# Optimization experiments

Measured on AMD Instinct MI355X. Metric: run time of the kernel, lower is better.

The kernel has to match this reference:

```python
import jax, jax.numpy as jnp
import numpy as np

B, S, H, DH = 8, 2048, 4, 32
D = H * DH  # all_head_size = true_hidden_size = 128


def setup_inputs() -> dict:
    key = jax.random.key(0)
    ks = jax.random.split(key, 9)
    inp = {
        "query_tensor": jax.random.normal(ks[0], (B, S, D), dtype=jnp.float32),
        "key_tensor": jax.random.normal(ks[1], (B, S, D), dtype=jnp.float32),
        "value_tensor": jax.random.normal(ks[2], (B, S, D), dtype=jnp.float32),
        "attention_mask": jnp.zeros((B, 1, 1, S), dtype=jnp.float32),
        "head_mask": jnp.ones((1, H, 1, 1), dtype=jnp.float32),
        "Wq": jax.random.normal(ks[3], (D, D), dtype=jnp.float32) * 0.02,
        "bq": jnp.zeros((D,), dtype=jnp.float32),
        "Wk": jax.random.normal(ks[4], (D, D), dtype=jnp.float32) * 0.02,
        "bk": jnp.zeros((D,), dtype=jnp.float32),
        "Wv": jax.random.normal(ks[5], (D, D), dtype=jnp.float32) * 0.02,
        "bv": jnp.zeros((D,), dtype=jnp.float32),
    }
    return inp


def _split_heads(x):
    # (B, S, D) -> (B, H, S, DH)
    return x.reshape(B, S, H, DH).transpose(0, 2, 1, 3)


def reference(query_tensor, key_tensor, value_tensor, attention_mask, head_mask,
              Wq, bq, Wk, bk, Wv, bv):
    q = _split_heads(query_tensor @ Wq + bq)   # (B,H,S,DH)
    k = _split_heads(key_tensor @ Wk + bk)
    v = _split_heads(value_tensor @ Wv + bv)

    scale = 1.0 / jnp.sqrt(jnp.float32(DH))
    scores = jnp.einsum("bhqd,bhkd->bhqk", q, k) * scale + attention_mask
    probs = jax.nn.softmax(scores, axis=-1)
    # dropout is identity at inference (training=False)
    probs = probs * head_mask
    ctx = jnp.einsum("bhqk,bhkd->bhqd", probs, v)  # (B,H,S,DH)
    ctx = ctx.transpose(0, 2, 1, 3).reshape(B, S, D)
    return ctx
```

## Files before the change

### kernel.cpp

```cpp
#include <hip/hip_runtime.h>
#include <hip/hip_bf16.h>
#include <math.h>

#define B_ 8
#define S_ 2048
#define H_ 4
#define DH_ 32
#define D_ 128
#define BS_ (B_ * S_)
#define LOG2E 1.4426950408889634f
#define QSCALE (0.17677669529663687f * LOG2E)

typedef float f32x4  __attribute__((ext_vector_type(4)));
typedef float f32x16 __attribute__((ext_vector_type(16)));
typedef short s16x8  __attribute__((ext_vector_type(8)));

__device__ __forceinline__ unsigned short bf(float x) {
    return __builtin_bit_cast(unsigned short, __float2bfloat16(x));
}
__device__ __forceinline__ float bf2f(unsigned short u) {
    return __builtin_bit_cast(float, (unsigned int)u << 16);
}
__device__ __forceinline__ unsigned int pk2(float a, float b) {
    unsigned int r;
    asm("v_cvt_pk_bf16_f32 %0, %1, %2" : "=v"(r) : "v"(a), "v"(b));
    return r;
}
__device__ __forceinline__ void pswap(unsigned int& a, unsigned int& b) {
    asm volatile("v_permlane32_swap_b32 %0, %1" : "+v"(a), "+v"(b));
}
__device__ __forceinline__ void gll16(const void* g, void* l) {
    __builtin_amdgcn_global_load_lds(
        (const __attribute__((address_space(1))) unsigned int*)(g),
        (__attribute__((address_space(3))) unsigned int*)(l), 16, 0, 0);
}

#define OFF_Q  0u
#define OFF_K  2097152u
#define OFF_V  4194304u
#define OFF_W  6291456u
#define OFF_E  6389760u

__global__ __launch_bounds__(256) void wprep(
    const float* __restrict__ Wq, const float* __restrict__ Wk, const float* __restrict__ Wv,
    const float* __restrict__ maskg,
    unsigned short* __restrict__ Wt, unsigned short* __restrict__ Em)
{
    if (blockIdx.z == 3) {
        const int id16 = blockIdx.y * 4 + blockIdx.x;
        const int base = id16 * 1024 + threadIdx.x * 4;
        float4 m4 = *(const float4*)&maskg[base];
        ushort4 o;
        o.x = bf(__builtin_amdgcn_exp2f(m4.x * LOG2E));
        o.y = bf(__builtin_amdgcn_exp2f(m4.y * LOG2E));
        o.z = bf(__builtin_amdgcn_exp2f(m4.z * LOG2E));
        o.w = bf(__builtin_amdgcn_exp2f(m4.w * LOG2E));
        *(ushort4*)&Em[base] = o;
        return;
    }
    const float* W = (blockIdx.z == 0) ? Wq : (blockIdx.z == 1) ? Wk : Wv;
    unsigned short* Oh = Wt + (size_t)blockIdx.z * D_ * D_;
    unsigned short* Ol = Oh + 3 * D_ * D_;
    __shared__ float tf[32][36];
    const int t = threadIdx.x;
    const int kt = blockIdx.x * 32, ct = blockIdx.y * 32;
    {
        int kl = t >> 3, cl = (t & 7) * 4;
        float4 w4 = *(const float4*)&W[(size_t)(kt + kl) * D_ + ct + cl];
        tf[kl][cl + 0] = w4.x; tf[kl][cl + 1] = w4.y;
        tf[kl][cl + 2] = w4.z; tf[kl][cl + 3] = w4.w;
    }
    __syncthreads();
    {
        int cl = t >> 3, kl = (t & 7) * 4;
        ushort4 oh, ol;
        float v;
        v = tf[kl + 0][cl]; oh.x = bf(v); ol.x = bf(v - bf2f(oh.x));
        v = tf[kl + 1][cl]; oh.y = bf(v); ol.y = bf(v - bf2f(oh.y));
        v = tf[kl + 2][cl]; oh.z = bf(v); ol.z = bf(v - bf2f(oh.z));
        v = tf[kl + 3][cl]; oh.w = bf(v); ol.w = bf(v - bf2f(oh.w));
        *(ushort4*)&Oh[(size_t)(ct + cl) * D_ + kt + kl] = oh;
        *(ushort4*)&Ol[(size_t)(ct + cl) * D_ + kt + kl] = ol;
    }
}

__global__ __launch_bounds__(256) void qkv_mfma(
    const float* __restrict__ Xq, const float* __restrict__ Xk, const float* __restrict__ Xv,
    const unsigned short* __restrict__ Wt, const float* __restrict__ maskg,
    const float* __restrict__ bq, const float* __restrict__ bk, const float* __restrict__ bv,
    unsigned short* __restrict__ Qo, unsigned short* __restrict__ Kf,
    unsigned short* __restrict__ Vf)
{
    const int mode = blockIdx.z, chalf = blockIdx.y;
    const float* X; const float* bias; float scl;
    if (mode == 0)      { X = Xq; bias = bq; scl = QSCALE; }
    else if (mode == 1) { X = Xk; bias = bk; scl = 1.f; }
    else                { X = Xv; bias = bv; scl = 1.f; }
    const unsigned short* WmH = Wt + (size_t)mode * D_ * D_;
    const unsigned short* WmL = WmH + 3 * D_ * D_;

    __shared__ __align__(16) unsigned short xa[2 * 32 * 136];
    __shared__ __align__(16) unsigned short wt[2 * 64 * 136];

    const int t = threadIdx.x;
    const int w = t >> 6, lane = t & 63, lo = lane & 15, hi = lane >> 4;
    const int mf = w >> 1, nb = (w & 1) * 2;

    #pragma unroll
    for (int j = 0; j < 8; j++) {
        int idx = t + 256 * j;
        int part = idx >> 10, i2 = idx & 1023;
        int r = i2 >> 4, c16 = i2 & 15;
        const unsigned short* src = part ? WmL : WmH;
        uint4 v = *(const uint4*)&src[(size_t)(chalf * 64 + r) * D_ + c16 * 8];
        *(uint4*)&wt[part * 8704 + r * 136 + c16 * 8] = v;
    }

    for (int rt = 0; rt < 4; rt++) {
        const long row0 = ((long)blockIdx.x * 4 + rt) * 32;

        __syncthreads();
        #pragma unroll
        for (int j = 0; j < 4; j++) {
            int idx = t + 256 * j;
            int r = idx >> 5, c4 = idx & 31;
            float4 v = *(const float4*)(X + (row0 + r) * D_ + c4 * 4);
            ushort4 ph, pl;
            ph.x = bf(v.x); pl.x = bf(v.x - bf2f(ph.x));
            ph.y = bf(v.y); pl.y = bf(v.y - bf2f(ph.y));
            ph.z = bf(v.z); pl.z = bf(v.z - bf2f(ph.z));
            ph.w = bf(v.w); pl.w = bf(v.w - bf2f(ph.w));
            *(ushort4*)&xa[r * 136 + c4 * 4] = ph;
            *(ushort4*)&xa[4352 + r * 136 + c4 * 4] = pl;
        }
        __syncthreads();

        f32x4 acc[2] = {};
        #pragma unroll
        for (int kk = 0; kk < 4; kk++) {
            const int ko = kk * 32 + hi * 8;
            s16x8 ah = *(const s16x8*)&xa[(mf * 16 + lo) * 136 + ko];
            s16x8 al = *(const s16x8*)&xa[4352 + (mf * 16 + lo) * 136 + ko];
            #pragma unroll
            for (int n2 = 0; n2 < 2; n2++) {
                const int nf = nb + n2;
                s16x8 bh2 = *(const s16x8*)&wt[(nf * 16 + lo) * 136 + ko];
                s16x8 bl2 = *(const s16x8*)&wt[8704 + (nf * 16 + lo) * 136 + ko];
                acc[n2] = __builtin_amdgcn_mfma_f32_16x16x32_bf16(ah, bh2, acc[n2], 0, 0, 0);
                acc[n2] = __builtin_amdgcn_mfma_f32_16x16x32_bf16(al, bh2, acc[n2], 0, 0, 0);
                acc[n2] = __builtin_amdgcn_mfma_f32_16x16x32_bf16(ah, bl2, acc[n2], 0, 0, 0);
            }
        }
        __syncthreads();

        const long b_i = row0 >> 11;
        const long s0g = row0 & 2047;

        if (mode < 2) {
            #pragma unroll
            for (int n2 = 0; n2 < 2; n2++) {
                int c_l = (nb + n2) * 16 + lo;
                float bb = bias[chalf * 64 + c_l];
                #pragma unroll
                for (int r = 0; r < 4; r++) {
                    int s = mf * 16 + hi * 4 + r;
                    xa[s * 72 + c_l] = bf((acc[n2][r] + bb) * scl);
                }
            }
            __syncthreads();
            int s = t >> 3, part = t & 7;
            int c_g = chalf * 64 + part * 8;
            int h = c_g >> 5, dd = c_g & 31;
            long s_i = s0g + s;
            int bh = (int)(b_i * H_ + h);
            uint4 val = *(const uint4*)&xa[s * 72 + part * 8];
            if (mode == 0) {
                *(uint4*)(Qo + ((size_t)bh * S_ + s_i) * DH_ + dd) = val;
            } else {
                int fr = dd >> 4, hwd = (dd >> 3) & 1;
                size_t off = ((((size_t)bh * 64 + (s_i >> 5)) * 2 + fr) * 64
                              + (s_i & 31) + hwd * 32) * 8;
                *(uint4*)(Kf + off) = val;
            }
        } else {
            float emr[4];
            #pragma unroll
            for (int r = 0; r < 4; r++) {
                const int s_l = mf * 16 + hi * 4 + r;
                emr[r] = __builtin_amdgcn_exp2f(maskg[b_i * S_ + s0g + s_l] * LOG2E);
            }
            #pragma unroll
            for (int n2 = 0; n2 < 2; n2++) {
                int c_l = (nb + n2) * 16 + lo;
                float bb = bias[chalf * 64 + c_l];
                #pragma unroll
                for (int r = 0; r < 4; r++) {
                    int s = mf * 16 + hi * 4 + r;
                    xa[c_l * 68 + s] = bf((acc[n2][r] + bb) * emr[r]);
                }
            }
            __syncthreads();
            if (t < 128) {
                int c_l = t >> 1, sh2 = (t & 1) * 16;
                int c_g = chalf * 64 + c_l;
                int h = c_g >> 5, dd = c_g & 31;
                long key0 = s0g + sh2;
                int bh = (int)(b_i * H_ + h);
                size_t base = (((size_t)bh * 128 + (key0 >> 4)) * 64 + dd) * 8;
                uint2 p0 = *(const uint2*)&xa[c_l * 68 + sh2 + 0];
                uint2 p1 = *(const uint2*)&xa[c_l * 68 + sh2 + 4];
                uint2 p2 = *(const uint2*)&xa[c_l * 68 + sh2 + 8];
                uint2 p3 = *(const uint2*)&xa[c_l * 68 + sh2 + 12];
                *(uint4*)(Vf + base)       = make_uint4(p0.x, p0.y, p1.x, p1.y);
                *(uint4*)(Vf + base + 256) = make_uint4(p2.x, p2.y, p3.x, p3.y);
            }
        }
    }
}

__global__ __launch_bounds__(512) void flash_mfma(
    const unsigned short* __restrict__ Qg, const unsigned short* __restrict__ Kfg,
    const unsigned short* __restrict__ Vfg, const unsigned short* __restrict__ Emg,
    const float* __restrict__ head_mask, float* __restrict__ Out)
{
    __shared__ __align__(16) unsigned short smem[26624];

    const int t = threadIdx.x, w = t >> 6, lane = t & 63;
    const int l31 = lane & 31, hw = lane >> 5;
    const int kq = w & 3, qh = w >> 2;

    const int lid = blockIdx.x;
    const int xcd = lid & 7, ser = lid >> 3;
    const int bh = xcd * 4 + (ser >> 5);
    const int qi = ser & 31;
    const int b = bh >> 2, h = bh & 3;
    const int q0 = qi * 64 + qh * 32;

    *(uint2*)&smem[24576 + t * 4] = *(const uint2*)(Emg + (size_t)b * S_ + t * 4);

    const unsigned short* qp = Qg + ((size_t)bh * S_ + q0 + l31) * DH_ + hw * 8;
    const s16x8 qf0 = *(const s16x8*)qp;
    const s16x8 qf1 = *(const s16x8*)(qp + 16);

    const size_t kvbase = (size_t)bh * 65536;
    const unsigned short* ksrc = Kfg + kvbase + (size_t)w * 512 + (size_t)lane * 8;
    const unsigned short* vsrc = Vfg + kvbase + (size_t)w * 512 + (size_t)lane * 8;

    #pragma unroll
    for (int p = 0; p < 3; p++) {
        gll16(ksrc + (size_t)p * 4096, &smem[p * 4096 + w * 512]);
        gll16(vsrc + (size_t)p * 4096, &smem[12288 + p * 4096 + w * 512]);
    }
    __syncthreads();

    const unsigned short* emb = &smem[24576];
    f32x16 ctx = {}, lacc = {};
    const f32x16 z16 = {};

    s16x8 vf_cur0, vf_cur1, ef_cur0, ef_cur1;
    f32x16 s_cur;
    {
        const unsigned short* kb = &smem[kq * 1024];
        const unsigned short* vb = &smem[12288 + kq * 1024];
        s16x8 k0 = *(const s16x8*)(kb + (size_t)lane * 8);
        s16x8 k1 = *(const s16x8*)(kb + 512 + (size_t)lane * 8);
        vf_cur0 = *(const s16x8*)(vb + (size_t)lane * 8);
        vf_cur1 = *(const s16x8*)(vb + 512 + (size_t)lane * 8);
        ef_cur0 = *(const s16x8*)(emb + kq * 32 + hw * 8);
        ef_cur1 = *(const s16x8*)(emb + kq * 32 + hw * 8 + 16);
        s_cur = __builtin_amdgcn_mfma_f32_32x32x16_bf16(k0, qf0, z16, 0, 0, 0);
        s_cur = __builtin_amdgcn_mfma_f32_32x32x16_bf16(k1, qf1, s_cur, 0, 0, 0);
    }

    #pragma unroll
    for (int tile = 0; tile < 16; tile++) {
        if (tile < 14)       { asm volatile("s_waitcnt vmcnt(2)" ::: "memory"); }
        else if (tile == 14) { asm volatile("s_waitcnt vmcnt(0)" ::: "memory"); }
        __builtin_amdgcn_sched_barrier(0);
        __builtin_amdgcn_s_barrier();
        __builtin_amdgcn_sched_barrier(0);

        f32x16 s_next;
        s16x8 vf_n0, vf_n1, ef_n0, ef_n1;
        if (tile < 15) {
            const int nb3 = ((tile + 1) % 3) * 4096 + kq * 1024;
            const unsigned short* kb = &smem[nb3];
            const unsigned short* vb = &smem[12288 + nb3];
            s16x8 kn0 = *(const s16x8*)(kb + (size_t)lane * 8);
            s16x8 kn1 = *(const s16x8*)(kb + 512 + (size_t)lane * 8);
            vf_n0 = *(const s16x8*)(vb + (size_t)lane * 8);
            vf_n1 = *(const s16x8*)(vb + 512 + (size_t)lane * 8);
            ef_n0 = *(const s16x8*)(emb + (tile + 1) * 128 + kq * 32 + hw * 8);
            ef_n1 = *(const s16x8*)(emb + (tile + 1) * 128 + kq * 32 + hw * 8 + 16);
            s_next = __builtin_amdgcn_mfma_f32_32x32x16_bf16(kn0, qf0, z16, 0, 0, 0);
            s_next = __builtin_amdgcn_mfma_f32_32x32x16_bf16(kn1, qf1, s_next, 0, 0, 0);

            if (tile <= 12) {
                gll16(ksrc + (size_t)(tile + 3) * 4096, &smem[(tile % 3) * 4096 + w * 512]);
                gll16(vsrc + (size_t)(tile + 3) * 4096, &smem[12288 + (tile % 3) * 4096 + w * 512]);
            }
        }

        unsigned int pd[8];
        #pragma unroll
        for (int j = 0; j < 8; j++) {
            pd[j] = pk2(__builtin_amdgcn_exp2f(s_cur[2 * j]),
                        __builtin_amdgcn_exp2f(s_cur[2 * j + 1]));
        }
        pswap(pd[0], pd[2]); pswap(pd[1], pd[3]);
        pswap(pd[4], pd[6]); pswap(pd[5], pd[7]);
        const s16x8 pa0 = __builtin_bit_cast(s16x8, make_uint4(pd[0], pd[1], pd[2], pd[3]));
        const s16x8 pa1 = __builtin_bit_cast(s16x8, make_uint4(pd[4], pd[5], pd[6], pd[7]));

        ctx  = __builtin_amdgcn_mfma_f32_32x32x16_bf16(pa0, vf_cur0, ctx, 0, 0, 0);
        lacc = __builtin_amdgcn_mfma_f32_32x32x16_bf16(pa0, ef_cur0, lacc, 0, 0, 0);
        ctx  = __builtin_amdgcn_mfma_f32_32x32x16_bf16(pa1, vf_cur1, ctx, 0, 0, 0);
        lacc = __builtin_amdgcn_mfma_f32_32x32x16_bf16(pa1, ef_cur1, lacc, 0, 0, 0);

        if (tile < 15) {
            s_cur = s_next;
            vf_cur0 = vf_n0; vf_cur1 = vf_n1;
            ef_cur0 = ef_n0; ef_cur1 = ef_n1;
        }
    }

    __syncthreads();
    float* ms = (float*)smem;
    #define MS(qh_, sl_, ln_, r_) ms[(((qh_) * 2 + (sl_)) * 64 + (ln_)) * 33 + (r_)]

    if (kq >= 2) {
        #pragma unroll
        for (int r = 0; r < 16; r++) {
            MS(qh, kq - 2, lane, r) = ctx[r];
            MS(qh, kq - 2, lane, 16 + r) = lacc[r];
        }
    }
    __syncthreads();
    if (kq < 2) {
        #pragma unroll
        for (int r = 0; r < 16; r++) {
            ctx[r]  += MS(qh, kq, lane, r);
            lacc[r] += MS(qh, kq, lane, 16 + r);
        }
    }
    __syncthreads();
    if (kq == 1) {
        #pragma unroll
        for (int r = 0; r < 16; r++) {
            MS(qh, 0, lane, r) = ctx[r];
            MS(qh, 0, lane, 16 + r) = lacc[r];
        }
    }
    __syncthreads();
    if (kq == 0) {
        #pragma unroll
        for (int r = 0; r < 16; r++) {
            ctx[r]  += MS(qh, 0, lane, r);
            lacc[r] += MS(qh, 0, lane, 16 + r);
        }
        const float hm = head_mask[h];
        #pragma unroll
        for (int r = 0; r < 16; r++) {
            const int qrow = (r & 3) + 8 * (r >> 2) + 4 * hw;
            Out[((size_t)b * S_ + q0 + qrow) * D_ + h * DH_ + l31] = ctx[r] * hm / lacc[r];
        }
    }
    #undef MS
}

extern "C" void kernel_launch(void* const* d_in, const int* in_sizes, int n_in,
                              void* d_out, int out_size, void* d_ws, size_t ws_size,
                              hipStream_t stream) {
    const float* Xq   = (const float*)d_in[0];
    const float* Xk   = (const float*)d_in[1];
    const float* Xv   = (const float*)d_in[2];
    const float* mask = (const float*)d_in[3];
    const float* hm   = (const float*)d_in[4];
    const float* Wq   = (const float*)d_in[5];
    const float* bq   = (const float*)d_in[6];
    const float* Wk   = (const float*)d_in[7];
    const float* bk   = (const float*)d_in[8];
    const float* Wv   = (const float*)d_in[9];
    const float* bv   = (const float*)d_in[10];
    float* out = (float*)d_out;

    unsigned short* ws = (unsigned short*)d_ws;
    unsigned short* Qo = ws + OFF_Q;
    unsigned short* Kf = ws + OFF_K;
    unsigned short* Vf = ws + OFF_V;
    unsigned short* Wt = ws + OFF_W;
    unsigned short* Em = ws + OFF_E;

    wprep<<<dim3(4, 4, 4), 256, 0, stream>>>(Wq, Wk, Wv, mask, Wt, Em);
    qkv_mfma<<<dim3(128, 2, 3), 256, 0, stream>>>(Xq, Xk, Xv, Wt, mask,
                                                  bq, bk, bv, Qo, Kf, Vf);
    flash_mfma<<<dim3(1024), 512, 0, stream>>>(Qo, Kf, Vf, Em, hm, out);
}
```

Before: 52.68 us.

## Rebalance flash kernel to 4 query groups x 2 key splits per block

Changes the flash attention block decomposition from 2 query subgroups x 4 key-split waves to 4 query subgroups x 2 key-split waves, so each block covers 128 queries and the grid halves to 512 blocks. Each K/V tile staged in shared memory is now reused by twice as many query rows, which halves global K/V traffic per output and cuts LDS use. The cross-wave reduction drops from two stages to one. In exchange, each wave runs twice as many key tiles (32) in a loop that is no longer unrolled, and there are fewer blocks to fill the GPU.

```diff
diff --git a/kernel.cpp b/kernel.cpp
--- a/kernel.cpp
+++ b/kernel.cpp
@@ -223,37 +223,37 @@
     const unsigned short* __restrict__ Vfg, const unsigned short* __restrict__ Emg,
     const float* __restrict__ head_mask, float* __restrict__ Out)
 {
-    __shared__ __align__(16) unsigned short smem[26624];
+    __shared__ __align__(16) unsigned short smem[16896];
 
     const int t = threadIdx.x, w = t >> 6, lane = t & 63;
     const int l31 = lane & 31, hw = lane >> 5;
-    const int kq = w & 3, qh = w >> 2;
+    const int kq = w & 1, qh = w >> 1;
 
     const int lid = blockIdx.x;
     const int xcd = lid & 7, ser = lid >> 3;
-    const int bh = xcd * 4 + (ser >> 5);
-    const int qi = ser & 31;
+    const int bh = xcd * 4 + (ser >> 4);
+    const int qi = ser & 15;
     const int b = bh >> 2, h = bh & 3;
-    const int q0 = qi * 64 + qh * 32;
-
-    *(uint2*)&smem[24576 + t * 4] = *(const uint2*)(Emg + (size_t)b * S_ + t * 4);
+    const int q0 = qi * 128 + qh * 32;
+
+    *(uint2*)&smem[12288 + t * 4] = *(const uint2*)(Emg + (size_t)b * S_ + t * 4);
 
     const unsigned short* qp = Qg + ((size_t)bh * S_ + q0 + l31) * DH_ + hw * 8;
     const s16x8 qf0 = *(const s16x8*)qp;
     const s16x8 qf1 = *(const s16x8*)(qp + 16);
 
     const size_t kvbase = (size_t)bh * 65536;
-    const unsigned short* ksrc = Kfg + kvbase + (size_t)w * 512 + (size_t)lane * 8;
-    const unsigned short* vsrc = Vfg + kvbase + (size_t)w * 512 + (size_t)lane * 8;
+    const int schunk = w & 3;
+    const unsigned short* ssrc = ((w < 4) ? Kfg : Vfg) + kvbase
+                               + (size_t)schunk * 512 + (size_t)lane * 8;
+    const int sdst = ((w < 4) ? 0 : 6144) + schunk * 512;
 
     #pragma unroll
-    for (int p = 0; p < 3; p++) {
-        gll16(ksrc + (size_t)p * 4096, &smem[p * 4096 + w * 512]);
-        gll16(vsrc + (size_t)p * 4096, &smem[12288 + p * 4096 + w * 512]);
-    }
+    for (int p = 0; p < 3; p++)
+        gll16(ssrc + (size_t)p * 2048, &smem[p * 2048 + sdst]);
     __syncthreads();
 
-    const unsigned short* emb = &smem[24576];
+    const unsigned short* emb = &smem[12288];
     f32x16 ctx = {}, lacc = {};
     const f32x16 z16 = {};
 
@@ -261,7 +261,7 @@
     f32x16 s_cur;
     {
         const unsigned short* kb = &smem[kq * 1024];
-        const unsigned short* vb = &smem[12288 + kq * 1024];
+        const unsigned short* vb = &smem[6144 + kq * 1024];
         s16x8 k0 = *(const s16x8*)(kb + (size_t)lane * 8);
         s16x8 k1 = *(const s16x8*)(kb + 512 + (size_t)lane * 8);
         vf_cur0 = *(const s16x8*)(vb + (size_t)lane * 8);
@@ -272,33 +272,30 @@
         s_cur = __builtin_amdgcn_mfma_f32_32x32x16_bf16(k1, qf1, s_cur, 0, 0, 0);
     }
 
-    #pragma unroll
-    for (int tile = 0; tile < 16; tile++) {
-        if (tile < 14)       { asm volatile("s_waitcnt vmcnt(2)" ::: "memory"); }
-        else if (tile == 14) { asm volatile("s_waitcnt vmcnt(0)" ::: "memory"); }
+    for (int tile = 0; tile < 32; tile++) {
+        if (tile < 30)       { asm volatile("s_waitcnt vmcnt(1)" ::: "memory"); }
+        else if (tile == 30) { asm volatile("s_waitcnt vmcnt(0)" ::: "memory"); }
         __builtin_amdgcn_sched_barrier(0);
         __builtin_amdgcn_s_barrier();
         __builtin_amdgcn_sched_barrier(0);
 
         f32x16 s_next;
         s16x8 vf_n0, vf_n1, ef_n0, ef_n1;
-        if (tile < 15) {
-            const int nb3 = ((tile + 1) % 3) * 4096 + kq * 1024;
+        if (tile < 31) {
+            const int nb3 = ((tile + 1) % 3) * 2048 + kq * 1024;
             const unsigned short* kb = &smem[nb3];
-            const unsigned short* vb = &smem[12288 + nb3];
+            const unsigned short* vb = &smem[6144 + nb3];
             s16x8 kn0 = *(const s16x8*)(kb + (size_t)lane * 8);
             s16x8 kn1 = *(const s16x8*)(kb + 512 + (size_t)lane * 8);
             vf_n0 = *(const s16x8*)(vb + (size_t)lane * 8);
             vf_n1 = *(const s16x8*)(vb + 512 + (size_t)lane * 8);
-            ef_n0 = *(const s16x8*)(emb + (tile + 1) * 128 + kq * 32 + hw * 8);
-            ef_n1 = *(const s16x8*)(emb + (tile + 1) * 128 + kq * 32 + hw * 8 + 16);
+            ef_n0 = *(const s16x8*)(emb + (tile + 1) * 64 + kq * 32 + hw * 8);
+            ef_n1 = *(const s16x8*)(emb + (tile + 1) * 64 + kq * 32 + hw * 8 + 16);
             s_next = __builtin_amdgcn_mfma_f32_32x32x16_bf16(kn0, qf0, z16, 0, 0, 0);
             s_next = __builtin_amdgcn_mfma_f32_32x32x16_bf16(kn1, qf1, s_next, 0, 0, 0);
 
-            if (tile <= 12) {
-                gll16(ksrc + (size_t)(tile + 3) * 4096, &smem[(tile % 3) * 4096 + w * 512]);
-                gll16(vsrc + (size_t)(tile + 3) * 4096, &smem[12288 + (tile % 3) * 4096 + w * 512]);
-            }
+            if (tile <= 28)
+                gll16(ssrc + (size_t)(tile + 3) * 2048, &smem[(tile % 3) * 2048 + sdst]);
         }
 
         unsigned int pd[8];
@@ -317,7 +314,7 @@
         ctx  = __builtin_amdgcn_mfma_f32_32x32x16_bf16(pa1, vf_cur1, ctx, 0, 0, 0);
         lacc = __builtin_amdgcn_mfma_f32_32x32x16_bf16(pa1, ef_cur1, lacc, 0, 0, 0);
 
-        if (tile < 15) {
+        if (tile < 31) {
             s_cur = s_next;
             vf_cur0 = vf_n0; vf_cur1 = vf_n1;
             ef_cur0 = ef_n0; ef_cur1 = ef_n1;
@@ -326,37 +323,21 @@
 
     __syncthreads();
     float* ms = (float*)smem;
-    #define MS(qh_, sl_, ln_, r_) ms[(((qh_) * 2 + (sl_)) * 64 + (ln_)) * 33 + (r_)]
-
-    if (kq >= 2) {
+    #define MS(qh_, ln_, r_) ms[((qh_) * 64 + (ln_)) * 33 + (r_)]
+
+    if (kq == 1) {
         #pragma unroll
         for (int r = 0; r < 16; r++) {
-            MS(qh, kq - 2, lane, r) = ctx[r];
-            MS(qh, kq - 2, lane, 16 + r) = lacc[r];
-        }
-    }
-    __syncthreads();
-    if (kq < 2) {
-        #pragma unroll
-        for (int r = 0; r < 16; r++) {
-            ctx[r]  += MS(qh, kq, lane, r);
-            lacc[r] += MS(qh, kq, lane, 16 + r);
-        }
-    }
-    __syncthreads();
-    if (kq == 1) {
-        #pragma unroll
-        for (int r = 0; r < 16; r++) {
-            MS(qh, 0, lane, r) = ctx[r];
-            MS(qh, 0, lane, 16 + r) = lacc[r];
+            MS(qh, lane, r) = ctx[r];
+            MS(qh, lane, 16 + r) = lacc[r];
         }
     }
     __syncthreads();
     if (kq == 0) {
         #pragma unroll
         for (int r = 0; r < 16; r++) {
-            ctx[r]  += MS(qh, 0, lane, r);
-            lacc[r] += MS(qh, 0, lane, 16 + r);
+            ctx[r]  += MS(qh, lane, r);
+            lacc[r] += MS(qh, lane, 16 + r);
         }
         const float hm = head_mask[h];
         #pragma unroll
@@ -394,5 +375,5 @@
     wprep<<<dim3(4, 4, 4), 256, 0, stream>>>(Wq, Wk, Wv, mask, Wt, Em);
     qkv_mfma<<<dim3(128, 2, 3), 256, 0, stream>>>(Xq, Xk, Xv, Wt, mask,
                                                   bq, bk, bv, Qo, Kf, Vf);
-    flash_mfma<<<dim3(1024), 512, 0, stream>>>(Qo, Kf, Vf, Em, hm, out);
-}
+    flash_mfma<<<dim3(512), 512, 0, stream>>>(Qo, Kf, Vf, Em, hm, out);
+}
```

New measurement: 52.92 us. About the same (+0.5%).

## Process two query sub-tiles per wave to reuse K/V tiles and halve blocks

Applied to the files above, without the earlier changes.

Each wave now handles 64 query rows as two 32-row sub-tiles that share the same K, V and mask fragments loaded from LDS. The grid shrinks from 1024 to 512 blocks, so each K/V tile is streamed into LDS half as often. The software pipelining that computed the next tile's scores early is removed in favour of two independent score/exp/PV chains per tile, which the scheduler can interleave. The cost is higher register pressure, fewer blocks to fill the GPU, and a reduction epilogue that now runs twice with extra barriers.

```diff
diff --git a/kernel.cpp b/kernel.cpp
--- a/kernel.cpp
+++ b/kernel.cpp
@@ -227,20 +227,23 @@
 
     const int t = threadIdx.x, w = t >> 6, lane = t & 63;
     const int l31 = lane & 31, hw = lane >> 5;
-    const int kq = w & 3, qh = w >> 2;
+    const int kq = w & 3, qw = w >> 2;
 
     const int lid = blockIdx.x;
     const int xcd = lid & 7, ser = lid >> 3;
-    const int bh = xcd * 4 + (ser >> 5);
-    const int qi = ser & 31;
+    const int bh = xcd * 4 + (ser >> 4);
+    const int qi = ser & 15;
     const int b = bh >> 2, h = bh & 3;
-    const int q0 = qi * 64 + qh * 32;
+    const int q0 = qi * 128 + qw * 64;
 
     *(uint2*)&smem[24576 + t * 4] = *(const uint2*)(Emg + (size_t)b * S_ + t * 4);
 
-    const unsigned short* qp = Qg + ((size_t)bh * S_ + q0 + l31) * DH_ + hw * 8;
-    const s16x8 qf0 = *(const s16x8*)qp;
-    const s16x8 qf1 = *(const s16x8*)(qp + 16);
+    const unsigned short* qpA = Qg + ((size_t)bh * S_ + q0 + l31) * DH_ + hw * 8;
+    const unsigned short* qpB = qpA + 32 * DH_;
+    const s16x8 qfA0 = *(const s16x8*)qpA;
+    const s16x8 qfA1 = *(const s16x8*)(qpA + 16);
+    const s16x8 qfB0 = *(const s16x8*)qpB;
+    const s16x8 qfB1 = *(const s16x8*)(qpB + 16);
 
     const size_t kvbase = (size_t)bh * 65536;
     const unsigned short* ksrc = Kfg + kvbase + (size_t)w * 512 + (size_t)lane * 8;
@@ -254,116 +257,120 @@
     __syncthreads();
 
     const unsigned short* emb = &smem[24576];
-    f32x16 ctx = {}, lacc = {};
+    f32x16 ctxA = {}, ctxB = {}, laccA = {}, laccB = {};
     const f32x16 z16 = {};
-
-    s16x8 vf_cur0, vf_cur1, ef_cur0, ef_cur1;
-    f32x16 s_cur;
-    {
-        const unsigned short* kb = &smem[kq * 1024];
-        const unsigned short* vb = &smem[12288 + kq * 1024];
-        s16x8 k0 = *(const s16x8*)(kb + (size_t)lane * 8);
-        s16x8 k1 = *(const s16x8*)(kb + 512 + (size_t)lane * 8);
-        vf_cur0 = *(const s16x8*)(vb + (size_t)lane * 8);
-        vf_cur1 = *(const s16x8*)(vb + 512 + (size_t)lane * 8);
-        ef_cur0 = *(const s16x8*)(emb + kq * 32 + hw * 8);
-        ef_cur1 = *(const s16x8*)(emb + kq * 32 + hw * 8 + 16);
-        s_cur = __builtin_amdgcn_mfma_f32_32x32x16_bf16(k0, qf0, z16, 0, 0, 0);
-        s_cur = __builtin_amdgcn_mfma_f32_32x32x16_bf16(k1, qf1, s_cur, 0, 0, 0);
-    }
 
     #pragma unroll
     for (int tile = 0; tile < 16; tile++) {
         if (tile < 14)       { asm volatile("s_waitcnt vmcnt(2)" ::: "memory"); }
-        else if (tile == 14) { asm volatile("s_waitcnt vmcnt(0)" ::: "memory"); }
+        else                 { asm volatile("s_waitcnt vmcnt(0)" ::: "memory"); }
         __builtin_amdgcn_sched_barrier(0);
         __builtin_amdgcn_s_barrier();
         __builtin_amdgcn_sched_barrier(0);
 
-        f32x16 s_next;
-        s16x8 vf_n0, vf_n1, ef_n0, ef_n1;
-        if (tile < 15) {
-            const int nb3 = ((tile + 1) % 3) * 4096 + kq * 1024;
-            const unsigned short* kb = &smem[nb3];
-            const unsigned short* vb = &smem[12288 + nb3];
-            s16x8 kn0 = *(const s16x8*)(kb + (size_t)lane * 8);
-            s16x8 kn1 = *(const s16x8*)(kb + 512 + (size_t)lane * 8);
-            vf_n0 = *(const s16x8*)(vb + (size_t)lane * 8);
-            vf_n1 = *(const s16x8*)(vb + 512 + (size_t)lane * 8);
-            ef_n0 = *(const s16x8*)(emb + (tile + 1) * 128 + kq * 32 + hw * 8);
-            ef_n1 = *(const s16x8*)(emb + (tile + 1) * 128 + kq * 32 + hw * 8 + 16);
-            s_next = __builtin_amdgcn_mfma_f32_32x32x16_bf16(kn0, qf0, z16, 0, 0, 0);
-            s_next = __builtin_amdgcn_mfma_f32_32x32x16_bf16(kn1, qf1, s_next, 0, 0, 0);
-
-            if (tile <= 12) {
-                gll16(ksrc + (size_t)(tile + 3) * 4096, &smem[(tile % 3) * 4096 + w * 512]);
-                gll16(vsrc + (size_t)(tile + 3) * 4096, &smem[12288 + (tile % 3) * 4096 + w * 512]);
-            }
-        }
-
-        unsigned int pd[8];
-        #pragma unroll
-        for (int j = 0; j < 8; j++) {
-            pd[j] = pk2(__builtin_amdgcn_exp2f(s_cur[2 * j]),
-                        __builtin_amdgcn_exp2f(s_cur[2 * j + 1]));
-        }
-        pswap(pd[0], pd[2]); pswap(pd[1], pd[3]);
-        pswap(pd[4], pd[6]); pswap(pd[5], pd[7]);
-        const s16x8 pa0 = __builtin_bit_cast(s16x8, make_uint4(pd[0], pd[1], pd[2], pd[3]));
-        const s16x8 pa1 = __builtin_bit_cast(s16x8, make_uint4(pd[4], pd[5], pd[6], pd[7]));
-
-        ctx  = __builtin_amdgcn_mfma_f32_32x32x16_bf16(pa0, vf_cur0, ctx, 0, 0, 0);
-        lacc = __builtin_amdgcn_mfma_f32_32x32x16_bf16(pa0, ef_cur0, lacc, 0, 0, 0);
-        ctx  = __builtin_amdgcn_mfma_f32_32x32x16_bf16(pa1, vf_cur1, ctx, 0, 0, 0);
-        lacc = __builtin_amdgcn_mfma_f32_32x32x16_bf16(pa1, ef_cur1, lacc, 0, 0, 0);
-
-        if (tile < 15) {
-            s_cur = s_next;
-            vf_cur0 = vf_n0; vf_cur1 = vf_n1;
-            ef_cur0 = ef_n0; ef_cur1 = ef_n1;
+        const int nb3 = (tile % 3) * 4096 + kq * 1024;
+        const unsigned short* kb = &smem[nb3];
+        const unsigned short* vb = &smem[12288 + nb3];
+        const s16x8 kf0 = *(const s16x8*)(kb + (size_t)lane * 8);
+        const s16x8 kf1 = *(const s16x8*)(kb + 512 + (size_t)lane * 8);
+        const s16x8 vf0 = *(const s16x8*)(vb + (size_t)lane * 8);
+        const s16x8 vf1 = *(const s16x8*)(vb + 512 + (size_t)lane * 8);
+        const s16x8 ef0 = *(const s16x8*)(emb + tile * 128 + kq * 32 + hw * 8);
+        const s16x8 ef1 = *(const s16x8*)(emb + tile * 128 + kq * 32 + hw * 8 + 16);
+
+        if (tile <= 12) {
+            gll16(ksrc + (size_t)(tile + 3) * 4096, &smem[(tile % 3) * 4096 + w * 512]);
+            gll16(vsrc + (size_t)(tile + 3) * 4096, &smem[12288 + (tile % 3) * 4096 + w * 512]);
+        }
+        asm volatile("s_waitcnt lgkmcnt(0)" ::: "memory");
+        __builtin_amdgcn_sched_barrier(0);
+
+        {
+            f32x16 s = __builtin_amdgcn_mfma_f32_32x32x16_bf16(kf0, qfA0, z16, 0, 0, 0);
+            s = __builtin_amdgcn_mfma_f32_32x32x16_bf16(kf1, qfA1, s, 0, 0, 0);
+            unsigned int pd[8];
+            #pragma unroll
+            for (int j = 0; j < 8; j++) {
+                pd[j] = pk2(__builtin_amdgcn_exp2f(s[2 * j]),
+                            __builtin_amdgcn_exp2f(s[2 * j + 1]));
+            }
+            pswap(pd[0], pd[2]); pswap(pd[1], pd[3]);
+            pswap(pd[4], pd[6]); pswap(pd[5], pd[7]);
+            const s16x8 pa0 = __builtin_bit_cast(s16x8, make_uint4(pd[0], pd[1], pd[2], pd[3]));
+            const s16x8 pa1 = __builtin_bit_cast(s16x8, make_uint4(pd[4], pd[5], pd[6], pd[7]));
+            ctxA  = __builtin_amdgcn_mfma_f32_32x32x16_bf16(pa0, vf0, ctxA, 0, 0, 0);
+            laccA = __builtin_amdgcn_mfma_f32_32x32x16_bf16(pa0, ef0, laccA, 0, 0, 0);
+            ctxA  = __builtin_amdgcn_mfma_f32_32x32x16_bf16(pa1, vf1, ctxA, 0, 0, 0);
+            laccA = __builtin_amdgcn_mfma_f32_32x32x16_bf16(pa1, ef1, laccA, 0, 0, 0);
+        }
+        {
+            f32x16 s = __builtin_amdgcn_mfma_f32_32x32x16_bf16(kf0, qfB0, z16, 0, 0, 0);
+            s = __builtin_amdgcn_mfma_f32_32x32x16_bf16(kf1, qfB1, s, 0, 0, 0);
+            unsigned int pd[8];
+            #pragma unroll
+            for (int j = 0; j < 8; j++) {
+                pd[j] = pk2(__builtin_amdgcn_exp2f(s[2 * j]),
+                            __builtin_amdgcn_exp2f(s[2 * j + 1]));
+            }
+            pswap(pd[0], pd[2]); pswap(pd[1], pd[3]);
+            pswap(pd[4], pd[6]); pswap(pd[5], pd[7]);
+            const s16x8 pa0 = __builtin_bit_cast(s16x8, make_uint4(pd[0], pd[1], pd[2], pd[3]));
+            const s16x8 pa1 = __builtin_bit_cast(s16x8, make_uint4(pd[4], pd[5], pd[6], pd[7]));
+            ctxB  = __builtin_amdgcn_mfma_f32_32x32x16_bf16(pa0, vf0, ctxB, 0, 0, 0);
+            laccB = __builtin_amdgcn_mfma_f32_32x32x16_bf16(pa0, ef0, laccB, 0, 0, 0);
+            ctxB  = __builtin_amdgcn_mfma_f32_32x32x16_bf16(pa1, vf1, ctxB, 0, 0, 0);
+            laccB = __builtin_amdgcn_mfma_f32_32x32x16_bf16(pa1, ef1, laccB, 0, 0, 0);
         }
     }
 
     __syncthreads();
     float* ms = (float*)smem;
-    #define MS(qh_, sl_, ln_, r_) ms[(((qh_) * 2 + (sl_)) * 64 + (ln_)) * 33 + (r_)]
-
-    if (kq >= 2) {
-        #pragma unroll
-        for (int r = 0; r < 16; r++) {
-            MS(qh, kq - 2, lane, r) = ctx[r];
-            MS(qh, kq - 2, lane, 16 + r) = lacc[r];
-        }
-    }
-    __syncthreads();
-    if (kq < 2) {
-        #pragma unroll
-        for (int r = 0; r < 16; r++) {
-            ctx[r]  += MS(qh, kq, lane, r);
-            lacc[r] += MS(qh, kq, lane, 16 + r);
-        }
-    }
-    __syncthreads();
-    if (kq == 1) {
-        #pragma unroll
-        for (int r = 0; r < 16; r++) {
-            MS(qh, 0, lane, r) = ctx[r];
-            MS(qh, 0, lane, 16 + r) = lacc[r];
-        }
-    }
-    __syncthreads();
-    if (kq == 0) {
-        #pragma unroll
-        for (int r = 0; r < 16; r++) {
-            ctx[r]  += MS(qh, 0, lane, r);
-            lacc[r] += MS(qh, 0, lane, 16 + r);
-        }
-        const float hm = head_mask[h];
-        #pragma unroll
-        for (int r = 0; r < 16; r++) {
-            const int qrow = (r & 3) + 8 * (r >> 2) + 4 * hw;
-            Out[((size_t)b * S_ + q0 + qrow) * D_ + h * DH_ + l31] = ctx[r] * hm / lacc[r];
-        }
+    #define MS(qw_, sl_, ln_, r_) ms[(((qw_) * 2 + (sl_)) * 64 + (ln_)) * 33 + (r_)]
+    const float hm = head_mask[h];
+
+    #pragma unroll
+    for (int sub = 0; sub < 2; sub++) {
+        f32x16& ctx  = sub ? ctxB : ctxA;
+        f32x16& lacc = sub ? laccB : laccA;
+        const int qs = q0 + sub * 32;
+
+        if (kq >= 2) {
+            #pragma unroll
+            for (int r = 0; r < 16; r++) {
+                MS(qw, kq - 2, lane, r) = ctx[r];
+                MS(qw, kq - 2, lane, 16 + r) = lacc[r];
+            }
+        }
+        __syncthreads();
+        if (kq < 2) {
+            #pragma unroll
+            for (int r = 0; r < 16; r++) {
+                ctx[r]  += MS(qw, kq, lane, r);
+                lacc[r] += MS(qw, kq, lane, 16 + r);
+            }
+        }
+        __syncthreads();
+        if (kq == 1) {
+            #pragma unroll
+            for (int r = 0; r < 16; r++) {
+                MS(qw, 0, lane, r) = ctx[r];
+                MS(qw, 0, lane, 16 + r) = lacc[r];
+            }
+        }
+        __syncthreads();
+        if (kq == 0) {
+            #pragma unroll
+            for (int r = 0; r < 16; r++) {
+                ctx[r]  += MS(qw, 0, lane, r);
+                lacc[r] += MS(qw, 0, lane, 16 + r);
+            }
+            #pragma unroll
+            for (int r = 0; r < 16; r++) {
+                const int qrow = (r & 3) + 8 * (r >> 2) + 4 * hw;
+                Out[((size_t)b * S_ + qs + qrow) * D_ + h * DH_ + l31] = ctx[r] * hm / lacc[r];
+            }
+        }
+        __syncthreads();
     }
     #undef MS
 }
@@ -394,5 +401,5 @@
     wprep<<<dim3(4, 4, 4), 256, 0, stream>>>(Wq, Wk, Wv, mask, Wt, Em);
     qkv_mfma<<<dim3(128, 2, 3), 256, 0, stream>>>(Xq, Xk, Xv, Wt, mask,
                                                   bq, bk, bv, Qo, Kf, Vf);
-    flash_mfma<<<dim3(1024), 512, 0, stream>>>(Qo, Kf, Vf, Em, hm, out);
-}
+    flash_mfma<<<dim3(512), 512, 0, stream>>>(Qo, Kf, Vf, Em, hm, out);
+}
```

Result: slower. 54.37 us (+3.2%).
